# Kernel tuning notes

Hardware: AMD Instinct MI355X
Metric: run time of the kernel (lower is better)

Reference implementation:

```python
import jax, jax.numpy as jnp
import numpy as np

N_NODES = 50000
N_EDGES = 800000
D_FEAT = 128
UNITS = 128


def setup_inputs() -> dict:
    key = jax.random.key(0)
    k1, k2, k3, k4 = jax.random.split(key, 4)
    x = jax.random.normal(k1, (N_NODES, D_FEAT), dtype=jnp.float32)
    source = jax.random.randint(k2, (N_EDGES,), 0, N_NODES, dtype=jnp.int32)
    target = jax.random.randint(k3, (N_EDGES,), 0, N_NODES, dtype=jnp.int32)
    W = jax.random.normal(k4, (D_FEAT, UNITS), dtype=jnp.float32) * (1.0 / np.sqrt(D_FEAT))
    b = jnp.zeros((UNITS,), dtype=jnp.float32)
    return {"x": x, "source": source, "target": target, "W": W, "b": b}


def _degree(idx, n_nodes):
    # in/out degree = segment-sum of unit edge weights; clamp to >= 1 (no self loops)
    deg = jnp.zeros((n_nodes,), dtype=jnp.float32).at[idx].add(1.0)
    return jnp.maximum(deg, 1.0)


def reference(x, source, target, W, b):
    n = x.shape[0]
    # degree_normalization == "in_out": sender scale from out-degree, receiver from in-degree
    sender_scale = jax.lax.rsqrt(_degree(source, n))[:, None]      # [N, 1]
    receiver_scale = jax.lax.rsqrt(_degree(target, n))[:, None]    # [N, 1]
    normalized = sender_scale * x                                  # [N, D]
    source_bcast = normalized[source]                              # [E, D] gather
    pooled = jax.ops.segment_sum(source_bcast, target, num_segments=n)  # [N, D] scatter-add
    pooled = receiver_scale * pooled
    # Dense(units, activation='relu', use_bias=True)
    return jax.nn.relu(pooled @ W + b)
```

## Files before the change

### kernel.cpp

```cpp
#include <hip/hip_runtime.h>
#include <hip/hip_bf16.h>

#define N_FEAT 128
#define EPT 8
#define CHUNK 2048
#define BSHIFT 8
#define MAXRANGE 256

typedef short bf16x8 __attribute__((ext_vector_type(8)));
typedef float f32x4  __attribute__((ext_vector_type(4)));

__device__ __forceinline__ unsigned short f2bf_rtne(float f) {
    unsigned u = __float_as_uint(f);
    u += 0x7fffu + ((u >> 16) & 1u);
    return (unsigned short)(u >> 16);
}

__global__ __launch_bounds__(256) void count_kernel(const int* __restrict__ source,
                                                    const int* __restrict__ target,
                                                    int* __restrict__ countsT,
                                                    int E, int NB, int NBLK) {
    __shared__ int ht[MAXRANGE];
    __shared__ int hs[MAXRANGE];
    int tid = threadIdx.x, b = blockIdx.x;
    ht[tid] = 0; hs[tid] = 0;
    __syncthreads();
    int base = b * CHUNK;
    #pragma unroll
    for (int j = 0; j < EPT; ++j) {
        int e = base + j * 256 + tid;
        if (e < E) {
            atomicAdd(&ht[target[e] >> BSHIFT], 1);
            atomicAdd(&hs[source[e] >> BSHIFT], 1);
        }
    }
    __syncthreads();
    int M = NB * NBLK;
    for (int k = tid; k < NB; k += 256) {
        countsT[k * NBLK + b]     = ht[k];
        countsT[M + k * NBLK + b] = hs[k];
    }
}

__global__ void block_reduce_kernel(const int* __restrict__ v,
                                    int* __restrict__ bsum, int M) {
    __shared__ int sb[256];
    int tid = threadIdx.x;
    int i = blockIdx.x * 256 + tid;
    sb[tid] = (i < M) ? v[i] : 0;
    __syncthreads();
    #pragma unroll
    for (int off = 128; off > 0; off >>= 1) {
        if (tid < off) sb[tid] += sb[tid + off];
        __syncthreads();
    }
    if (tid == 0) bsum[blockIdx.x] = sb[0];
}

__global__ void scan_bsum_kernel(int* __restrict__ bsum, int nb) {
    __shared__ int sb[1024];
    int tid = threadIdx.x;
    int v = (tid < nb) ? bsum[tid] : 0;
    sb[tid] = v;
    __syncthreads();
    for (int off = 1; off < 1024; off <<= 1) {
        int t = (tid >= off) ? sb[tid - off] : 0;
        __syncthreads();
        sb[tid] += t;
        __syncthreads();
    }
    if (tid < nb) bsum[tid] = sb[tid] - v;
}

__global__ void scan_final_kernel(const int* __restrict__ v,
                                  const int* __restrict__ bsum,
                                  int* __restrict__ scanned, int M) {
    __shared__ int sb[256];
    int tid = threadIdx.x;
    int i = blockIdx.x * 256 + tid;
    int x = (i < M) ? v[i] : 0;
    sb[tid] = x;
    __syncthreads();
    #pragma unroll
    for (int off = 1; off < 256; off <<= 1) {
        int t = (tid >= off) ? sb[tid - off] : 0;
        __syncthreads();
        sb[tid] += t;
        __syncthreads();
    }
    if (i < M) scanned[i] = bsum[blockIdx.x] + sb[tid] - x;
}

__global__ __launch_bounds__(256) void scatter_kernel(const int* __restrict__ source,
                                                      const int* __restrict__ target,
                                                      const int* __restrict__ scanAll,
                                                      unsigned int* __restrict__ pairsT,
                                                      unsigned char* __restrict__ srcB,
                                                      int E, int NB, int NBLK) {
    __shared__ unsigned int  lds_pairs[CHUNK];
    __shared__ unsigned char lds_kt[CHUNK];
    __shared__ unsigned char lds_src[CHUNK];
    __shared__ unsigned char lds_ks[CHUNK];
    __shared__ int ct[MAXRANGE], cs[MAXRANGE];
    __shared__ int st[MAXRANGE], ss[MAXRANGE];
    __shared__ int gt[MAXRANGE], gs[MAXRANGE];
    int tid = threadIdx.x, b = blockIdx.x;
    int M = NB * NBLK;
    int base = b * CHUNK;
    int cnt = E - base; if (cnt > CHUNK) cnt = CHUNK;

    ct[tid] = 0; cs[tid] = 0;
    for (int k = tid; k < NB; k += 256) {
        gt[k] = scanAll[k * NBLK + b];
        gs[k] = scanAll[M + k * NBLK + b] - E;
    }
    __syncthreads();
    #pragma unroll
    for (int j = 0; j < EPT; ++j) {
        int e = base + j * 256 + tid;
        if (e < E) {
            atomicAdd(&ct[target[e] >> BSHIFT], 1);
            atomicAdd(&cs[source[e] >> BSHIFT], 1);
        }
    }
    __syncthreads();
    int vt = ct[tid], vs = cs[tid];
    st[tid] = vt; ss[tid] = vs;
    __syncthreads();
    #pragma unroll
    for (int off = 1; off < 256; off <<= 1) {
        int t1 = (tid >= off) ? st[tid - off] : 0;
        int t2 = (tid >= off) ? ss[tid - off] : 0;
        __syncthreads();
        st[tid] += t1; ss[tid] += t2;
        __syncthreads();
    }
    int et = st[tid] - vt, es = ss[tid] - vs;
    __syncthreads();
    st[tid] = et; ss[tid] = es;
    ct[tid] = et; cs[tid] = es;
    __syncthreads();
    #pragma unroll
    for (int j = 0; j < EPT; ++j) {
        int e = base + j * 256 + tid;
        if (e < E) {
            int t = target[e], s = source[e];
            int k = t >> BSHIFT;
            int p = atomicAdd(&ct[k], 1);
            lds_pairs[p] = (unsigned)s | ((unsigned)(t & 255) << 16);
            lds_kt[p] = (unsigned char)k;
            int k2 = s >> BSHIFT;
            int p2 = atomicAdd(&cs[k2], 1);
            lds_src[p2] = (unsigned char)(s & 255);
            lds_ks[p2] = (unsigned char)k2;
        }
    }
    __syncthreads();
    for (int i = tid; i < cnt; i += 256) {
        int k = lds_kt[i];
        pairsT[gt[k] + (i - st[k])] = lds_pairs[i];
        int k2 = lds_ks[i];
        srcB[gs[k2] + (i - ss[k2])] = lds_src[i];
    }
}

__global__ __launch_bounds__(256) void so_kernel(const unsigned char* __restrict__ srcB,
                                                 const int* __restrict__ scanAll,
                                                 float* __restrict__ so,
                                                 int N, int NB, int NBLK, int E) {
    __shared__ int hist[MAXRANGE];
    int b = blockIdx.x, tid = threadIdx.x;
    int M = NB * NBLK;
    hist[tid] = 0;
    __syncthreads();
    int start = scanAll[M + b * NBLK] - E;
    int end   = (b + 1 < NB) ? (scanAll[M + (b + 1) * NBLK] - E) : E;
    for (int i = start + tid; i < end; i += 256)
        atomicAdd(&hist[srcB[i]], 1);
    __syncthreads();
    int node = (b << BSHIFT) + tid;
    if (node < N) {
        int d = hist[tid]; if (d < 1) d = 1;
        so[node] = rsqrtf((float)d);
    }
}

__global__ __launch_bounds__(256) void prescale_kernel(const float* __restrict__ x,
                                                       const float* __restrict__ so,
                                                       unsigned short* __restrict__ xb,
                                                       int N) {
    int idx = blockIdx.x * 256 + threadIdx.x;
    int total = N * (N_FEAT / 4);
    if (idx >= total) return;
    int row = idx >> 5;
    float s = so[row];
    float4 v = ((const float4*)x)[idx];
    unsigned short o[4] = {f2bf_rtne(s * v.x), f2bf_rtne(s * v.y),
                           f2bf_rtne(s * v.z), f2bf_rtne(s * v.w)};
    ((ushort4*)xb)[idx] = make_ushort4(o[0], o[1], o[2], o[3]);
}

__global__ __launch_bounds__(256) void wpack_kernel(const float* __restrict__ W,
                                                    unsigned short* __restrict__ Whi,
                                                    unsigned short* __restrict__ Wlo) {
    int idx = blockIdx.x * 256 + threadIdx.x;
    int lane = idx & 63;
    int ks = (idx >> 6) & 3;
    int ct = idx >> 8;
    int n  = ct * 16 + (lane & 15);
    int k0 = ks * 32 + (lane >> 4) * 8;
    unsigned short h[8], l[8];
    #pragma unroll
    for (int j = 0; j < 8; ++j) {
        float w = W[(k0 + j) * N_FEAT + n];
        unsigned short hh = f2bf_rtne(w);
        float fh = __uint_as_float((unsigned)hh << 16);
        h[j] = hh;
        l[j] = f2bf_rtne(w - fh);
    }
    size_t off = (size_t)idx * 8;
    *(ushort4*)(Whi + off)     = make_ushort4(h[0], h[1], h[2], h[3]);
    *(ushort4*)(Whi + off + 4) = make_ushort4(h[4], h[5], h[6], h[7]);
    *(ushort4*)(Wlo + off)     = make_ushort4(l[0], l[1], l[2], l[3]);
    *(ushort4*)(Wlo + off + 4) = make_ushort4(l[4], l[5], l[6], l[7]);
}

__global__ __launch_bounds__(256) void csr_kernel(const unsigned int* __restrict__ pairsT,
                                                  const int* __restrict__ scanAll,
                                                  int* __restrict__ offsets,
                                                  int* __restrict__ elist,
                                                  float* __restrict__ ri,
                                                  int N, int NB, int NBLK, int E) {
    __shared__ int hist[MAXRANGE];
    __shared__ int sb[MAXRANGE];
    __shared__ int excl[MAXRANGE];
    __shared__ int cur[MAXRANGE];
    int b = blockIdx.x, tid = threadIdx.x;
    hist[tid] = 0; cur[tid] = 0;
    __syncthreads();
    int start = scanAll[b * NBLK];
    int end   = (b + 1 < NB) ? scanAll[(b + 1) * NBLK] : E;
    for (int i = start + tid; i < end; i += 256)
        atomicAdd(&hist[(pairsT[i] >> 16) & 255], 1);
    __syncthreads();
    int deg = hist[tid];
    sb[tid] = deg;
    __syncthreads();
    #pragma unroll
    for (int off = 1; off < 256; off <<= 1) {
        int t = (tid >= off) ? sb[tid - off] : 0;
        __syncthreads();
        sb[tid] += t;
        __syncthreads();
    }
    excl[tid] = sb[tid] - deg;
    __syncthreads();
    int node = (b << BSHIFT) + tid;
    if (node < N) {
        offsets[node] = start + excl[tid];
        int d = deg; if (d < 1) d = 1;
        ri[node] = rsqrtf((float)d);
    }
    if (b == 0 && tid == 0) offsets[N] = E;
    for (int i = start + tid; i < end; i += 256) {
        unsigned w = pairsT[i];
        int tl = (w >> 16) & 255;
        int pos = atomicAdd(&cur[tl], 1);
        elist[start + excl[tl] + pos] = (int)(w & 0xFFFFu);
    }
}

__global__ void agg_kernel(const unsigned short* __restrict__ xb,
                           const int* __restrict__ elist,
                           const int* __restrict__ offsets,
                           const float* __restrict__ ri,
                           float* __restrict__ pooled, int N) {
    int wave = (blockIdx.x * blockDim.x + threadIdx.x) >> 6;
    int lane = threadIdx.x & 63;
    if (wave >= N) return;
    int start = offsets[wave];
    int end   = offsets[wave + 1];
    int col = lane * 2;

    float2 a0 = make_float2(0.f, 0.f), a1 = a0, a2 = a0, a3 = a0;
    int i = start;
    for (; i + 8 <= end; i += 8) {
        int e0 = __builtin_amdgcn_readfirstlane(elist[i]);
        int e1 = __builtin_amdgcn_readfirstlane(elist[i + 1]);
        int e2 = __builtin_amdgcn_readfirstlane(elist[i + 2]);
        int e3 = __builtin_amdgcn_readfirstlane(elist[i + 3]);
        int e4 = __builtin_amdgcn_readfirstlane(elist[i + 4]);
        int e5 = __builtin_amdgcn_readfirstlane(elist[i + 5]);
        int e6 = __builtin_amdgcn_readfirstlane(elist[i + 6]);
        int e7 = __builtin_amdgcn_readfirstlane(elist[i + 7]);
        unsigned u0 = *(const unsigned*)(xb + (size_t)e0 * N_FEAT + col);
        unsigned u1 = *(const unsigned*)(xb + (size_t)e1 * N_FEAT + col);
        unsigned u2 = *(const unsigned*)(xb + (size_t)e2 * N_FEAT + col);
        unsigned u3 = *(const unsigned*)(xb + (size_t)e3 * N_FEAT + col);
        unsigned u4 = *(const unsigned*)(xb + (size_t)e4 * N_FEAT + col);
        unsigned u5 = *(const unsigned*)(xb + (size_t)e5 * N_FEAT + col);
        unsigned u6 = *(const unsigned*)(xb + (size_t)e6 * N_FEAT + col);
        unsigned u7 = *(const unsigned*)(xb + (size_t)e7 * N_FEAT + col);
        a0.x += __uint_as_float(u0 << 16); a0.y += __uint_as_float(u0 & 0xffff0000u);
        a1.x += __uint_as_float(u1 << 16); a1.y += __uint_as_float(u1 & 0xffff0000u);
        a2.x += __uint_as_float(u2 << 16); a2.y += __uint_as_float(u2 & 0xffff0000u);
        a3.x += __uint_as_float(u3 << 16); a3.y += __uint_as_float(u3 & 0xffff0000u);
        a0.x += __uint_as_float(u4 << 16); a0.y += __uint_as_float(u4 & 0xffff0000u);
        a1.x += __uint_as_float(u5 << 16); a1.y += __uint_as_float(u5 & 0xffff0000u);
        a2.x += __uint_as_float(u6 << 16); a2.y += __uint_as_float(u6 & 0xffff0000u);
        a3.x += __uint_as_float(u7 << 16); a3.y += __uint_as_float(u7 & 0xffff0000u);
    }
    for (; i < end; ++i) {
        int e = __builtin_amdgcn_readfirstlane(elist[i]);
        unsigned u = *(const unsigned*)(xb + (size_t)e * N_FEAT + col);
        a0.x += __uint_as_float(u << 16); a0.y += __uint_as_float(u & 0xffff0000u);
    }
    float r = ri[wave];
    float2 outv = make_float2(((a0.x + a1.x) + (a2.x + a3.x)) * r,
                              ((a0.y + a1.y) + (a2.y + a3.y)) * r);
    *(float2*)(&pooled[(size_t)wave * N_FEAT + col]) = outv;
}

__global__ __launch_bounds__(256) void gemm_mfma_kernel(const unsigned short* __restrict__ Whi,
                                                        const unsigned short* __restrict__ Wlo,
                                                        const float* __restrict__ bias,
                                                        float* __restrict__ P,
                                                        int N) {
    int wave = threadIdx.x >> 6;
    int lane = threadIdx.x & 63;
    int quad = lane >> 4;
    int rowbase = blockIdx.x * 64 + wave * 16;
    int m = rowbase + (lane & 15);
    int mload = (m < N) ? m : 0;

    bf16x8 Ahi[4], Alo[4];
    const float* prow = P + (size_t)mload * N_FEAT + quad * 8;
    #pragma unroll
    for (int ks = 0; ks < 4; ++ks) {
        float4 v0 = *(const float4*)(prow + ks * 32);
        float4 v1 = *(const float4*)(prow + ks * 32 + 4);
        float f[8] = {v0.x, v0.y, v0.z, v0.w, v1.x, v1.y, v1.z, v1.w};
        bf16x8 h, l;
        #pragma unroll
        for (int j = 0; j < 8; ++j) {
            unsigned short hh = f2bf_rtne(f[j]);
            h[j] = (short)hh;
            l[j] = (short)f2bf_rtne(f[j] - __uint_as_float((unsigned)hh << 16));
        }
        Ahi[ks] = h; Alo[ks] = l;
    }

    const bf16x8* BH = (const bf16x8*)Whi;
    const bf16x8* BL = (const bf16x8*)Wlo;

    #pragma unroll
    for (int ct = 0; ct < 8; ++ct) {
        f32x4 acc = {0.f, 0.f, 0.f, 0.f};
        #pragma unroll
        for (int ks = 0; ks < 4; ++ks) {
            bf16x8 bh = BH[(ct * 4 + ks) * 64 + lane];
            bf16x8 bl = BL[(ct * 4 + ks) * 64 + lane];
            acc = __builtin_amdgcn_mfma_f32_16x16x32_bf16(Ahi[ks], bh, acc, 0, 0, 0);
            acc = __builtin_amdgcn_mfma_f32_16x16x32_bf16(Alo[ks], bh, acc, 0, 0, 0);
            acc = __builtin_amdgcn_mfma_f32_16x16x32_bf16(Ahi[ks], bl, acc, 0, 0, 0);
        }
        int colc = ct * 16 + (lane & 15);
        float bv = bias[colc];
        #pragma unroll
        for (int reg = 0; reg < 4; ++reg) {
            int r = rowbase + quad * 4 + reg;
            if (r < N)
                P[(size_t)r * N_FEAT + colc] = fmaxf(acc[reg] + bv, 0.f);
        }
    }
}

extern "C" void kernel_launch(void* const* d_in, const int* in_sizes, int n_in,
                              void* d_out, int out_size, void* d_ws, size_t ws_size,
                              hipStream_t stream) {
    const float* x      = (const float*)d_in[0];
    const int*   source = (const int*)d_in[1];
    const int*   target = (const int*)d_in[2];
    const float* W      = (const float*)d_in[3];
    const float* bias   = (const float*)d_in[4];
    float*       out    = (float*)d_out;

    const int N = in_sizes[0] / N_FEAT;
    const int E = in_sizes[1];

    const int NB   = (N + MAXRANGE - 1) >> BSHIFT;
    const int NBLK = (E + CHUNK - 1) / CHUNK;
    const int M    = NB * NBLK;
    const int MALL = 2 * M;
    const int nb2  = (MALL + 255) / 256;

    uintptr_t p = (uintptr_t)d_ws;
    auto carve = [&](size_t bytes) {
        p = (p + 255) & ~(uintptr_t)255;
        uintptr_t r = p;
        p += bytes;
        return (void*)r;
    };
    int*            countsT = (int*)carve((size_t)MALL * sizeof(int));
    int*            scanAll = (int*)carve((size_t)MALL * sizeof(int));
    int*            bsum    = (int*)carve((size_t)nb2 * sizeof(int));
    unsigned int*   pairsT  = (unsigned int*)carve((size_t)E * sizeof(unsigned int));
    int*            elist   = (int*)carve((size_t)E * sizeof(int));
    unsigned char*  srcB    = (unsigned char*)elist;
    float*          so      = (float*)carve((size_t)N * sizeof(float));
    float*          ri      = (float*)carve((size_t)N * sizeof(float));
    int*            offsets = (int*)carve((size_t)(N + 1) * sizeof(int));
    unsigned short* xb      = (unsigned short*)carve((size_t)N * N_FEAT * sizeof(unsigned short));
    unsigned short* Whi     = (unsigned short*)carve((size_t)N_FEAT * N_FEAT * sizeof(unsigned short));
    unsigned short* Wlo     = (unsigned short*)carve((size_t)N_FEAT * N_FEAT * sizeof(unsigned short));
    (void)ws_size; (void)n_in; (void)out_size;

    count_kernel<<<NBLK, 256, 0, stream>>>(source, target, countsT, E, NB, NBLK);
    block_reduce_kernel<<<nb2, 256, 0, stream>>>(countsT, bsum, MALL);
    scan_bsum_kernel<<<1, 1024, 0, stream>>>(bsum, nb2);
    scan_final_kernel<<<nb2, 256, 0, stream>>>(countsT, bsum, scanAll, MALL);
    scatter_kernel<<<NBLK, 256, 0, stream>>>(source, target, scanAll, pairsT, srcB, E, NB, NBLK);
    so_kernel<<<NB, 256, 0, stream>>>(srcB, scanAll, so, N, NB, NBLK, E);
    prescale_kernel<<<(N * (N_FEAT / 4) + 255) / 256, 256, 0, stream>>>(x, so, xb, N);
    wpack_kernel<<<8, 256, 0, stream>>>(W, Whi, Wlo);
    csr_kernel<<<NB, 256, 0, stream>>>(pairsT, scanAll, offsets, elist, ri, N, NB, NBLK, E);
    agg_kernel<<<(N + 3) / 4, 256, 0, stream>>>(xb, elist, offsets, ri, out, N);
    gemm_mfma_kernel<<<(N + 63) / 64, 256, 0, stream>>>(Whi, Wlo, bias, out, N);
}
```

Measured before the change: 188.5 us.

## Replace per-block bucket scan with atomic bucket totals and fuse degree prescale

Swaps the per-block count matrix and its three-stage scan for global per-bucket totals gathered with atomics, a single small scan, and atomic cursor claiming in the scatter kernel. The scatter kernel stages source and target in LDS so the second pass does not reread global memory. The out-degree histogram and x prescale are merged into one kernel, and the aggregation kernel now writes bf16 hi/lo splits directly so the GEMM skips the fp32 pooled round trip. This removes several launches and memory passes, at the cost of a memset, nondeterministic bucket placement order, and an extra hi/lo buffer pair.

```diff
diff --git a/kernel.cpp b/kernel.cpp
--- a/kernel.cpp
+++ b/kernel.cpp
@@ -15,11 +15,15 @@
     u += 0x7fffu + ((u >> 16) & 1u);
     return (unsigned short)(u >> 16);
 }
+__device__ __forceinline__ float bf2f(unsigned short h) {
+    return __uint_as_float((unsigned)h << 16);
+}
 
 __global__ __launch_bounds__(256) void count_kernel(const int* __restrict__ source,
                                                     const int* __restrict__ target,
-                                                    int* __restrict__ countsT,
-                                                    int E, int NB, int NBLK) {
+                                                    int* __restrict__ totT,
+                                                    int* __restrict__ totS,
+                                                    int E, int NB) {
     __shared__ int ht[MAXRANGE];
     __shared__ int hs[MAXRANGE];
     int tid = threadIdx.x, b = blockIdx.x;
@@ -35,68 +39,49 @@
         }
     }
     __syncthreads();
-    int M = NB * NBLK;
-    for (int k = tid; k < NB; k += 256) {
-        countsT[k * NBLK + b]     = ht[k];
-        countsT[M + k * NBLK + b] = hs[k];
-    }
-}
-
-__global__ void block_reduce_kernel(const int* __restrict__ v,
-                                    int* __restrict__ bsum, int M) {
-    __shared__ int sb[256];
+    if (tid < NB) {
+        int vt = ht[tid], vs = hs[tid];
+        if (vt) atomicAdd(&totT[tid], vt);
+        if (vs) atomicAdd(&totS[tid], vs);
+    }
+}
+
+__global__ void scan196_kernel(const int* __restrict__ totT,
+                               const int* __restrict__ totS,
+                               int* __restrict__ baseT, int* __restrict__ baseS,
+                               int* __restrict__ curT,  int* __restrict__ curS,
+                               int NB, int E) {
+    __shared__ int sb[256], sb2[256];
     int tid = threadIdx.x;
-    int i = blockIdx.x * 256 + tid;
-    sb[tid] = (i < M) ? v[i] : 0;
-    __syncthreads();
-    #pragma unroll
-    for (int off = 128; off > 0; off >>= 1) {
-        if (tid < off) sb[tid] += sb[tid + off];
-        __syncthreads();
-    }
-    if (tid == 0) bsum[blockIdx.x] = sb[0];
-}
-
-__global__ void scan_bsum_kernel(int* __restrict__ bsum, int nb) {
-    __shared__ int sb[1024];
-    int tid = threadIdx.x;
-    int v = (tid < nb) ? bsum[tid] : 0;
-    sb[tid] = v;
-    __syncthreads();
-    for (int off = 1; off < 1024; off <<= 1) {
-        int t = (tid >= off) ? sb[tid - off] : 0;
-        __syncthreads();
-        sb[tid] += t;
-        __syncthreads();
-    }
-    if (tid < nb) bsum[tid] = sb[tid] - v;
-}
-
-__global__ void scan_final_kernel(const int* __restrict__ v,
-                                  const int* __restrict__ bsum,
-                                  int* __restrict__ scanned, int M) {
-    __shared__ int sb[256];
-    int tid = threadIdx.x;
-    int i = blockIdx.x * 256 + tid;
-    int x = (i < M) ? v[i] : 0;
-    sb[tid] = x;
+    int vT = (tid < NB) ? totT[tid] : 0;
+    int vS = (tid < NB) ? totS[tid] : 0;
+    sb[tid] = vT; sb2[tid] = vS;
     __syncthreads();
     #pragma unroll
     for (int off = 1; off < 256; off <<= 1) {
-        int t = (tid >= off) ? sb[tid - off] : 0;
-        __syncthreads();
-        sb[tid] += t;
-        __syncthreads();
-    }
-    if (i < M) scanned[i] = bsum[blockIdx.x] + sb[tid] - x;
+        int t1 = (tid >= off) ? sb[tid - off] : 0;
+        int t2 = (tid >= off) ? sb2[tid - off] : 0;
+        __syncthreads();
+        sb[tid] += t1; sb2[tid] += t2;
+        __syncthreads();
+    }
+    if (tid < NB) {
+        int eT = sb[tid] - vT, eS = sb2[tid] - vS;
+        baseT[tid] = eT; baseS[tid] = eS;
+        curT[tid]  = eT; curS[tid]  = eS;
+    }
+    if (tid == 0) { baseT[NB] = E; baseS[NB] = E; }
 }
 
 __global__ __launch_bounds__(256) void scatter_kernel(const int* __restrict__ source,
                                                       const int* __restrict__ target,
-                                                      const int* __restrict__ scanAll,
+                                                      int* __restrict__ curT,
+                                                      int* __restrict__ curS,
                                                       unsigned int* __restrict__ pairsT,
                                                       unsigned char* __restrict__ srcB,
-                                                      int E, int NB, int NBLK) {
+                                                      int E, int NB) {
+    __shared__ int lsrc[CHUNK];
+    __shared__ int ltgt[CHUNK];
     __shared__ unsigned int  lds_pairs[CHUNK];
     __shared__ unsigned char lds_kt[CHUNK];
     __shared__ unsigned char lds_src[CHUNK];
@@ -105,22 +90,20 @@
     __shared__ int st[MAXRANGE], ss[MAXRANGE];
     __shared__ int gt[MAXRANGE], gs[MAXRANGE];
     int tid = threadIdx.x, b = blockIdx.x;
-    int M = NB * NBLK;
     int base = b * CHUNK;
     int cnt = E - base; if (cnt > CHUNK) cnt = CHUNK;
 
     ct[tid] = 0; cs[tid] = 0;
-    for (int k = tid; k < NB; k += 256) {
-        gt[k] = scanAll[k * NBLK + b];
-        gs[k] = scanAll[M + k * NBLK + b] - E;
-    }
     __syncthreads();
     #pragma unroll
     for (int j = 0; j < EPT; ++j) {
-        int e = base + j * 256 + tid;
+        int idx = j * 256 + tid;
+        int e = base + idx;
         if (e < E) {
-            atomicAdd(&ct[target[e] >> BSHIFT], 1);
-            atomicAdd(&cs[source[e] >> BSHIFT], 1);
+            int s = source[e], t = target[e];
+            lsrc[idx] = s; ltgt[idx] = t;
+            atomicAdd(&ct[t >> BSHIFT], 1);
+            atomicAdd(&cs[s >> BSHIFT], 1);
         }
     }
     __syncthreads();
@@ -136,15 +119,21 @@
         __syncthreads();
     }
     int et = st[tid] - vt, es = ss[tid] - vs;
+    int gT = 0, gS = 0;
+    if (tid < NB) {
+        if (vt) gT = atomicAdd(&curT[tid], vt);
+        if (vs) gS = atomicAdd(&curS[tid], vs);
+    }
     __syncthreads();
     st[tid] = et; ss[tid] = es;
     ct[tid] = et; cs[tid] = es;
+    gt[tid] = gT; gs[tid] = gS;
     __syncthreads();
     #pragma unroll
     for (int j = 0; j < EPT; ++j) {
-        int e = base + j * 256 + tid;
-        if (e < E) {
-            int t = target[e], s = source[e];
+        int idx = j * 256 + tid;
+        if (idx < cnt) {
+            int s = lsrc[idx], t = ltgt[idx];
             int k = t >> BSHIFT;
             int p = atomicAdd(&ct[k], 1);
             lds_pairs[p] = (unsigned)s | ((unsigned)(t & 255) << 16);
@@ -164,40 +153,37 @@
     }
 }
 
-__global__ __launch_bounds__(256) void so_kernel(const unsigned char* __restrict__ srcB,
-                                                 const int* __restrict__ scanAll,
-                                                 float* __restrict__ so,
-                                                 int N, int NB, int NBLK, int E) {
+__global__ __launch_bounds__(256) void so_prescale_kernel(const unsigned char* __restrict__ srcB,
+                                                          const int* __restrict__ baseS,
+                                                          const float* __restrict__ x,
+                                                          unsigned short* __restrict__ xb,
+                                                          int N, int NB) {
     __shared__ int hist[MAXRANGE];
+    __shared__ float so_l[MAXRANGE];
     int b = blockIdx.x, tid = threadIdx.x;
-    int M = NB * NBLK;
     hist[tid] = 0;
     __syncthreads();
-    int start = scanAll[M + b * NBLK] - E;
-    int end   = (b + 1 < NB) ? (scanAll[M + (b + 1) * NBLK] - E) : E;
-    for (int i = start + tid; i < end; i += 256)
+    int s0 = baseS[b], s1 = baseS[b + 1];
+    for (int i = s0 + tid; i < s1; i += 256)
         atomicAdd(&hist[srcB[i]], 1);
     __syncthreads();
-    int node = (b << BSHIFT) + tid;
-    if (node < N) {
+    {
         int d = hist[tid]; if (d < 1) d = 1;
-        so[node] = rsqrtf((float)d);
-    }
-}
-
-__global__ __launch_bounds__(256) void prescale_kernel(const float* __restrict__ x,
-                                                       const float* __restrict__ so,
-                                                       unsigned short* __restrict__ xb,
-                                                       int N) {
-    int idx = blockIdx.x * 256 + threadIdx.x;
-    int total = N * (N_FEAT / 4);
-    if (idx >= total) return;
-    int row = idx >> 5;
-    float s = so[row];
-    float4 v = ((const float4*)x)[idx];
-    unsigned short o[4] = {f2bf_rtne(s * v.x), f2bf_rtne(s * v.y),
-                           f2bf_rtne(s * v.z), f2bf_rtne(s * v.w)};
-    ((ushort4*)xb)[idx] = make_ushort4(o[0], o[1], o[2], o[3]);
+        so_l[tid] = rsqrtf((float)d);
+    }
+    __syncthreads();
+    int row0 = b << BSHIFT;
+    int nrows = N - row0; if (nrows > 256) nrows = 256;
+    if (nrows <= 0) return;
+    int nf4 = nrows * (N_FEAT / 4);
+    const float4* xr = (const float4*)(x + (size_t)row0 * N_FEAT);
+    ushort4* xo = (ushort4*)(xb + (size_t)row0 * N_FEAT);
+    for (int i = tid; i < nf4; i += 256) {
+        float s = so_l[i >> 5];
+        float4 v = xr[i];
+        xo[i] = make_ushort4(f2bf_rtne(s * v.x), f2bf_rtne(s * v.y),
+                             f2bf_rtne(s * v.z), f2bf_rtne(s * v.w));
+    }
 }
 
 __global__ __launch_bounds__(256) void wpack_kernel(const float* __restrict__ W,
@@ -214,9 +200,8 @@
     for (int j = 0; j < 8; ++j) {
         float w = W[(k0 + j) * N_FEAT + n];
         unsigned short hh = f2bf_rtne(w);
-        float fh = __uint_as_float((unsigned)hh << 16);
         h[j] = hh;
-        l[j] = f2bf_rtne(w - fh);
+        l[j] = f2bf_rtne(w - bf2f(hh));
     }
     size_t off = (size_t)idx * 8;
     *(ushort4*)(Whi + off)     = make_ushort4(h[0], h[1], h[2], h[3]);
@@ -226,11 +211,11 @@
 }
 
 __global__ __launch_bounds__(256) void csr_kernel(const unsigned int* __restrict__ pairsT,
-                                                  const int* __restrict__ scanAll,
+                                                  const int* __restrict__ baseT,
                                                   int* __restrict__ offsets,
                                                   int* __restrict__ elist,
                                                   float* __restrict__ ri,
-                                                  int N, int NB, int NBLK, int E) {
+                                                  int N, int NB, int E) {
     __shared__ int hist[MAXRANGE];
     __shared__ int sb[MAXRANGE];
     __shared__ int excl[MAXRANGE];
@@ -238,8 +223,8 @@
     int b = blockIdx.x, tid = threadIdx.x;
     hist[tid] = 0; cur[tid] = 0;
     __syncthreads();
-    int start = scanAll[b * NBLK];
-    int end   = (b + 1 < NB) ? scanAll[(b + 1) * NBLK] : E;
+    int start = baseT[b];
+    int end   = baseT[b + 1];
     for (int i = start + tid; i < end; i += 256)
         atomicAdd(&hist[(pairsT[i] >> 16) & 255], 1);
     __syncthreads();
@@ -274,7 +259,9 @@
                            const int* __restrict__ elist,
                            const int* __restrict__ offsets,
                            const float* __restrict__ ri,
-                           float* __restrict__ pooled, int N) {
+                           unsigned int* __restrict__ poolhi,
+                           unsigned int* __restrict__ poollo,
+                           int N) {
     int wave = (blockIdx.x * blockDim.x + threadIdx.x) >> 6;
     int lane = threadIdx.x & 63;
     if (wave >= N) return;
@@ -316,15 +303,21 @@
         a0.x += __uint_as_float(u << 16); a0.y += __uint_as_float(u & 0xffff0000u);
     }
     float r = ri[wave];
-    float2 outv = make_float2(((a0.x + a1.x) + (a2.x + a3.x)) * r,
-                              ((a0.y + a1.y) + (a2.y + a3.y)) * r);
-    *(float2*)(&pooled[(size_t)wave * N_FEAT + col]) = outv;
-}
-
-__global__ __launch_bounds__(256) void gemm_mfma_kernel(const unsigned short* __restrict__ Whi,
+    float vx = ((a0.x + a1.x) + (a2.x + a3.x)) * r;
+    float vy = ((a0.y + a1.y) + (a2.y + a3.y)) * r;
+    unsigned short hx = f2bf_rtne(vx), hy = f2bf_rtne(vy);
+    unsigned short lx = f2bf_rtne(vx - bf2f(hx)), ly = f2bf_rtne(vy - bf2f(hy));
+    size_t o = (size_t)wave * (N_FEAT / 2) + lane;
+    poolhi[o] = (unsigned)hx | ((unsigned)hy << 16);
+    poollo[o] = (unsigned)lx | ((unsigned)ly << 16);
+}
+
+__global__ __launch_bounds__(256) void gemm_mfma_kernel(const unsigned short* __restrict__ poolhi,
+                                                        const unsigned short* __restrict__ poollo,
+                                                        const unsigned short* __restrict__ Whi,
                                                         const unsigned short* __restrict__ Wlo,
                                                         const float* __restrict__ bias,
-                                                        float* __restrict__ P,
+                                                        float* __restrict__ out,
                                                         int N) {
     int wave = threadIdx.x >> 6;
     int lane = threadIdx.x & 63;
@@ -334,20 +327,12 @@
     int mload = (m < N) ? m : 0;
 
     bf16x8 Ahi[4], Alo[4];
-    const float* prow = P + (size_t)mload * N_FEAT + quad * 8;
+    const unsigned short* ah = poolhi + (size_t)mload * N_FEAT + quad * 8;
+    const unsigned short* al = poollo + (size_t)mload * N_FEAT + quad * 8;
     #pragma unroll
     for (int ks = 0; ks < 4; ++ks) {
-        float4 v0 = *(const float4*)(prow + ks * 32);
-        float4 v1 = *(const float4*)(prow + ks * 32 + 4);
-        float f[8] = {v0.x, v0.y, v0.z, v0.w, v1.x, v1.y, v1.z, v1.w};
-        bf16x8 h, l;
-        #pragma unroll
-        for (int j = 0; j < 8; ++j) {
-            unsigned short hh = f2bf_rtne(f[j]);
-            h[j] = (short)hh;
-            l[j] = (short)f2bf_rtne(f[j] - __uint_as_float((unsigned)hh << 16));
-        }
-        Ahi[ks] = h; Alo[ks] = l;
+        Ahi[ks] = *(const bf16x8*)(ah + ks * 32);
+        Alo[ks] = *(const bf16x8*)(al + ks * 32);
     }
 
     const bf16x8* BH = (const bf16x8*)Whi;
@@ -370,7 +355,7 @@
         for (int reg = 0; reg < 4; ++reg) {
             int r = rowbase + quad * 4 + reg;
             if (r < N)
-                P[(size_t)r * N_FEAT + colc] = fmaxf(acc[reg] + bv, 0.f);
+                out[(size_t)r * N_FEAT + colc] = fmaxf(acc[reg] + bv, 0.f);
         }
     }
 }
@@ -390,9 +375,6 @@
 
     const int NB   = (N + MAXRANGE - 1) >> BSHIFT;
     const int NBLK = (E + CHUNK - 1) / CHUNK;
-    const int M    = NB * NBLK;
-    const int MALL = 2 * M;
-    const int nb2  = (MALL + 255) / 256;
 
     uintptr_t p = (uintptr_t)d_ws;
     auto carve = [&](size_t bytes) {
@@ -401,29 +383,35 @@
         p += bytes;
         return (void*)r;
     };
-    int*            countsT = (int*)carve((size_t)MALL * sizeof(int));
-    int*            scanAll = (int*)carve((size_t)MALL * sizeof(int));
-    int*            bsum    = (int*)carve((size_t)nb2 * sizeof(int));
+    int*            tots    = (int*)carve((size_t)2 * NB * sizeof(int));
+    int*            totT    = tots;
+    int*            totS    = tots + NB;
+    int*            baseT   = (int*)carve((size_t)(NB + 1) * sizeof(int));
+    int*            baseS   = (int*)carve((size_t)(NB + 1) * sizeof(int));
+    int*            curT    = (int*)carve((size_t)NB * sizeof(int));
+    int*            curS    = (int*)carve((size_t)NB * sizeof(int));
     unsigned int*   pairsT  = (unsigned int*)carve((size_t)E * sizeof(unsigned int));
     int*            elist   = (int*)carve((size_t)E * sizeof(int));
     unsigned char*  srcB    = (unsigned char*)elist;
-    float*          so      = (float*)carve((size_t)N * sizeof(float));
     float*          ri      = (float*)carve((size_t)N * sizeof(float));
     int*            offsets = (int*)carve((size_t)(N + 1) * sizeof(int));
     unsigned short* xb      = (unsigned short*)carve((size_t)N * N_FEAT * sizeof(unsigned short));
+    unsigned int*   poolhi  = (unsigned int*)carve((size_t)N * (N_FEAT / 2) * sizeof(unsigned int));
+    unsigned int*   poollo  = (unsigned int*)carve((size_t)N * (N_FEAT / 2) * sizeof(unsigned int));
     unsigned short* Whi     = (unsigned short*)carve((size_t)N_FEAT * N_FEAT * sizeof(unsigned short));
     unsigned short* Wlo     = (unsigned short*)carve((size_t)N_FEAT * N_FEAT * sizeof(unsigned short));
     (void)ws_size; (void)n_in; (void)out_size;
 
-    count_kernel<<<NBLK, 256, 0, stream>>>(source, target, countsT, E, NB, NBLK);
-    block_reduce_kernel<<<nb2, 256, 0, stream>>>(countsT, bsum, MALL);
-    scan_bsum_kernel<<<1, 1024, 0, stream>>>(bsum, nb2);
-    scan_final_kernel<<<nb2, 256, 0, stream>>>(countsT, bsum, scanAll, MALL);
-    scatter_kernel<<<NBLK, 256, 0, stream>>>(source, target, scanAll, pairsT, srcB, E, NB, NBLK);
-    so_kernel<<<NB, 256, 0, stream>>>(srcB, scanAll, so, N, NB, NBLK, E);
-    prescale_kernel<<<(N * (N_FEAT / 4) + 255) / 256, 256, 0, stream>>>(x, so, xb, N);
+    (void)hipMemsetAsync(tots, 0, (size_t)2 * NB * sizeof(int), stream);
+
+    count_kernel<<<NBLK, 256, 0, stream>>>(source, target, totT, totS, E, NB);
+    scan196_kernel<<<1, 256, 0, stream>>>(totT, totS, baseT, baseS, curT, curS, NB, E);
+    scatter_kernel<<<NBLK, 256, 0, stream>>>(source, target, curT, curS, pairsT, srcB, E, NB);
+    so_prescale_kernel<<<NB, 256, 0, stream>>>(srcB, baseS, x, xb, N, NB);
     wpack_kernel<<<8, 256, 0, stream>>>(W, Whi, Wlo);
-    csr_kernel<<<NB, 256, 0, stream>>>(pairsT, scanAll, offsets, elist, ri, N, NB, NBLK, E);
-    agg_kernel<<<(N + 3) / 4, 256, 0, stream>>>(xb, elist, offsets, ri, out, N);
-    gemm_mfma_kernel<<<(N + 63) / 64, 256, 0, stream>>>(Whi, Wlo, bias, out, N);
-}
+    csr_kernel<<<NB, 256, 0, stream>>>(pairsT, baseT, offsets, elist, ri, N, NB, E);
+    agg_kernel<<<(N + 3) / 4, 256, 0, stream>>>(xb, elist, offsets, ri, poolhi, poollo, N);
+    gemm_mfma_kernel<<<(N + 63) / 64, 256, 0, stream>>>(
+        (const unsigned short*)poolhi, (const unsigned short*)poollo,
+        Whi, Wlo, bias, out, N);
+}
```

Result: slower. 198.6 us (+5.4%).
